# Performance work log

Measured on AMD Instinct MI355X. Metric: run time of the kernel, lower is better.

## Reference

```python
import jax, jax.numpy as jnp
import numpy as np

N_NODES = 50000
N_EDGES = 800000
HIDDEN = 128
IN_DIM = 128
OUT_DIM = 1
N_LAYERS = 4
N_GRAPHS = 32
LN_EPS = 1e-5


def setup_inputs() -> dict:
    key = jax.random.key(0)
    ks = jax.random.split(key, 12)
    s = 1.0 / np.sqrt(HIDDEN)
    inp = {
        "x": jax.random.normal(ks[0], (N_NODES, IN_DIM), dtype=jnp.float32),
        "edge_index": jax.random.randint(ks[1], (2, N_EDGES), 0, N_NODES, dtype=jnp.int64),
        "batch": jnp.sort(jax.random.randint(ks[2], (N_NODES,), 0, N_GRAPHS, dtype=jnp.int64)),
        "W_emb": jax.random.normal(ks[3], (HIDDEN, IN_DIM), dtype=jnp.float32) * s,
        "b_emb": jax.random.normal(ks[4], (HIDDEN,), dtype=jnp.float32) * s,
        "W_layers": jax.random.normal(ks[5], (N_LAYERS, HIDDEN, HIDDEN), dtype=jnp.float32) * s,
        "b_layers": jax.random.normal(ks[6], (N_LAYERS, HIDDEN), dtype=jnp.float32) * s,
        "ln_gamma": 1.0 + 0.02 * jax.random.normal(ks[7], (N_LAYERS, HIDDEN), dtype=jnp.float32),
        "ln_beta": 0.02 * jax.random.normal(ks[8], (N_LAYERS, HIDDEN), dtype=jnp.float32),
        "W_out": jax.random.normal(ks[9], (OUT_DIM, HIDDEN), dtype=jnp.float32) * s,
    }
    return inp


def _layer_norm(x, gamma, beta):
    mu = jnp.mean(x, axis=-1, keepdims=True)
    var = jnp.mean(jnp.square(x - mu), axis=-1, keepdims=True)
    return (x - mu) * jax.lax.rsqrt(var + LN_EPS) * gamma + beta


def reference(x, edge_index, batch, W_emb, b_emb, W_layers, b_layers, ln_gamma, ln_beta, W_out):
    n = x.shape[0]
    # add self-loops (PyG GCNConv default)
    loop = jnp.arange(n, dtype=edge_index.dtype)
    row = jnp.concatenate([edge_index[0], loop])  # source nodes
    col = jnp.concatenate([edge_index[1], loop])  # target nodes
    # symmetric normalization: deg over targets
    deg = jax.ops.segment_sum(jnp.ones_like(col, dtype=x.dtype), col, num_segments=n)
    dis = jnp.where(deg > 0, jax.lax.rsqrt(jnp.maximum(deg, 1.0)), 0.0)
    norm = dis[row] * dis[col]  # [E+N]

    h = x @ W_emb.T + b_emb  # embedding layer
    for i in range(N_LAYERS):
        t = h @ W_layers[i].T                      # [N, H] linear first
        msg = t[row] * norm[:, None]               # gather + scale  [E+N, H]
        agg = jax.ops.segment_sum(msg, col, num_segments=n) + b_layers[i]
        h = _layer_norm(h + jax.nn.relu(agg), ln_gamma[i], ln_beta[i])

    out = h @ W_out.T                              # [N, OUT_DIM]
    sums = jax.ops.segment_sum(out, batch, num_segments=N_GRAPHS)
    cnts = jax.ops.segment_sum(jnp.ones((n,), out.dtype), batch, num_segments=N_GRAPHS)
    return sums / jnp.maximum(cnts, 1.0)[:, None]  # [N_GRAPHS, OUT_DIM]
```

## Files before the change

kernel.cpp:

```cpp
#include <hip/hip_runtime.h>
#include <hip/hip_fp16.h>

#define NN 50000
#define NE 800000
#define NH 128
#define NG 32
#define NL 4
#define NB 196
#define PREPB 320
#define HISTB 3125
#define NTILE 12500
#define WSLOT (NH * NH)

typedef __attribute__((ext_vector_type(8))) short bf16x8;
typedef __attribute__((ext_vector_type(4))) float f32x4;
typedef __attribute__((ext_vector_type(2))) float f32x2;

__device__ inline short f2bf(float x) {
  union { float f; unsigned u; } v;
  v.f = x;
  unsigned r = v.u + 0x7FFF + ((v.u >> 16) & 1);
  return (short)(r >> 16);
}
__device__ inline float bf2f(short s) {
  union { unsigned u; float f; } v;
  v.u = ((unsigned)(unsigned short)s) << 16;
  return v.f;
}

__device__ inline int pdw(int t, int quad) {
  return (((2 * t + (quad >> 1)) & 3) << 3) + ((t >> 1) << 1) + (quad & 1);
}

__device__ inline void fp8row_fma(float (&ag)[4][8], uint4 qa, uint4 qb,
                                  float w) {
  const unsigned dw[8] = {qa.x, qa.y, qa.z, qa.w, qb.x, qb.y, qb.z, qb.w};
#pragma unroll
  for (int ks = 0; ks < 4; ++ks) {
    f32x2 u0 = __builtin_amdgcn_cvt_pk_f32_fp8(dw[2 * ks], 0);
    f32x2 u1 = __builtin_amdgcn_cvt_pk_f32_fp8(dw[2 * ks], 1);
    f32x2 u2 = __builtin_amdgcn_cvt_pk_f32_fp8(dw[2 * ks + 1], 0);
    f32x2 u3 = __builtin_amdgcn_cvt_pk_f32_fp8(dw[2 * ks + 1], 1);
    ag[ks][0] += u0.x * w; ag[ks][1] += u0.y * w;
    ag[ks][2] += u1.x * w; ag[ks][3] += u1.y * w;
    ag[ks][4] += u2.x * w; ag[ks][5] += u2.y * w;
    ag[ks][6] += u3.x * w; ag[ks][7] += u3.y * w;
  }
}

__device__ inline int block_exscan(int v) {
  __shared__ int wsum[4];
  int tid = threadIdx.x, wave = tid >> 6, lane = tid & 63;
  int x = v;
#pragma unroll
  for (int off = 1; off < 64; off <<= 1) {
    int y = __shfl_up(x, off, 64);
    if (lane >= off) x += y;
  }
  if (lane == 63) wsum[wave] = x;
  __syncthreads();
  int wp = 0;
  if (wave > 0) wp += wsum[0];
  if (wave > 1) wp += wsum[1];
  if (wave > 2) wp += wsum[2];
  return wp + x - v;
}

__global__ __launch_bounds__(256) void prep_hist_kernel(
    const float* __restrict__ W_emb, const float* __restrict__ W_layers,
    short* __restrict__ hi, short* __restrict__ lo, const int* __restrict__ row,
    const int* __restrict__ col, int* __restrict__ cnt4,
    int* __restrict__ rank) {
  if (blockIdx.x < PREPB) {
    int i = blockIdx.x * 256 + threadIdx.x;
    if (i >= 5 * WSLOT) return;
    int slot = i >> 14, f = i & (WSLOT - 1);
    int j = f & 7, lane = (f >> 3) & 63, tt = (f >> 9) & 7, ks = f >> 12;
    int n = tt * 16 + (lane & 15);
    int k = ks * 32 + ((lane >> 4) & 3) * 8 + j;
    const float* W = slot ? (W_layers + (size_t)(slot - 1) * WSLOT) : W_emb;
    float x = W[n * NH + k];
    short hh = f2bf(x);
    hi[i] = hh;
    lo[i] = f2bf(x - bf2f(hh));
  } else {
    int e = (blockIdx.x - PREPB) * 256 + threadIdx.x;
    if (e < NE) {
      int s = row[e];
      int t = s / NTILE;
      rank[e] = atomicAdd(&cnt4[col[e] * 4 + t], 1);
    }
  }
}

__global__ __launch_bounds__(256) void scan1_kernel(const int* __restrict__ cnt4,
                                                    int* __restrict__ bsum,
                                                    float* __restrict__ dis,
                                                    int* __restrict__ deg) {
  int i = blockIdx.x * 256 + threadIdx.x;
  int v = 0;
  if (i < NN) {
    int4 c4 = *(const int4*)&cnt4[i * 4];
    v = c4.x + c4.y + c4.z + c4.w;
    deg[i] = v;
    dis[i] = rsqrtf((float)(v + 1));
  }
  int lane = threadIdx.x & 63;
  int s = v;
#pragma unroll
  for (int off = 32; off; off >>= 1) s += __shfl_down(s, off, 64);
  __shared__ int ws[4];
  if (lane == 0) ws[threadIdx.x >> 6] = s;
  __syncthreads();
  if (threadIdx.x == 0) bsum[blockIdx.x] = ws[0] + ws[1] + ws[2] + ws[3];
}

__global__ __launch_bounds__(256) void scan3b_kernel(const int* __restrict__ deg,
                                                     const int* __restrict__ bsum,
                                                     int* __restrict__ offs) {
  __shared__ int ws2[4];
  int tid = threadIdx.x;
  int b = blockIdx.x;
  int v = (tid < NB && tid < b) ? bsum[tid] : 0;
  int lane = tid & 63;
  int s = v;
#pragma unroll
  for (int off = 32; off; off >>= 1) s += __shfl_down(s, off, 64);
  if (lane == 0) ws2[tid >> 6] = s;
  __syncthreads();
  int bo = ws2[0] + ws2[1] + ws2[2] + ws2[3];
  int i = b * 256 + tid;
  int c = (i < NN) ? deg[i] : 0;
  int ex = block_exscan(c);
  if (i < NN) offs[i] = bo + ex;
}

__global__ __launch_bounds__(256) void fill_kernel(const int* __restrict__ row,
                                                   const int* __restrict__ col,
                                                   const int* __restrict__ rank,
                                                   const int* __restrict__ cnt4,
                                                   const float* __restrict__ dis,
                                                   const int* __restrict__ offs,
                                                   int2* __restrict__ csr) {
  int e = blockIdx.x * 256 + threadIdx.x;
  if (e < NE) {
    int d = col[e];
    int s = row[e];
    int t = s / NTILE;
    int4 c4 = *(const int4*)&cnt4[d * 4];
    int pre = (t > 0 ? c4.x : 0) + (t > 1 ? c4.y : 0) + (t > 2 ? c4.z : 0);
    int pos = offs[d] + pre + rank[e];
    csr[pos] = make_int2(s, __float_as_int(dis[s] * dis[d]));
  }
}

__global__ __launch_bounds__(512) void emb_gemm(const float* __restrict__ Xf,
                                                const short* __restrict__ Whi,
                                                const short* __restrict__ Wlo,
                                                const float* __restrict__ bias,
                                                __half* __restrict__ hnew,
                                                unsigned char* __restrict__ h8) {
  __shared__ short Wh[WSLOT];
  __shared__ short Wl[WSLOT];
  int tid = threadIdx.x;
#pragma unroll
  for (int i = tid * 8; i < WSLOT; i += 512 * 8) {
    *(bf16x8*)&Wh[i] = *(const bf16x8*)(Whi + i);
    *(bf16x8*)&Wl[i] = *(const bf16x8*)(Wlo + i);
  }
  __syncthreads();

  int wave = tid >> 6, lane = tid & 63;
  int quad = lane >> 4, r16 = lane & 15;
  int m0 = blockIdx.x * 128 + wave * 16;
  if (m0 >= NN) return;
  int mA = m0 + r16;

  f32x4 acc[8];
#pragma unroll
  for (int t = 0; t < 8; ++t) acc[t] = (f32x4){0.f, 0.f, 0.f, 0.f};

#pragma unroll
  for (int ks = 0; ks < 4; ++ks) {
    int klane = ks * 32 + quad * 8;
    const float* xr = Xf + (size_t)mA * NH + klane;
    float4 a0 = *(const float4*)xr;
    float4 a1 = *(const float4*)(xr + 4);
    float af[8] = {a0.x, a0.y, a0.z, a0.w, a1.x, a1.y, a1.z, a1.w};
    bf16x8 xhi, xlo;
#pragma unroll
    for (int j = 0; j < 8; ++j) {
      short h = f2bf(af[j]);
      xhi[j] = h;
      xlo[j] = f2bf(af[j] - bf2f(h));
    }
#pragma unroll
    for (int t = 0; t < 8; ++t) {
      int fidx = ((ks * 8 + t) * 64 + lane) << 3;
      bf16x8 whi = *(const bf16x8*)&Wh[fidx];
      bf16x8 wlo = *(const bf16x8*)&Wl[fidx];
      acc[t] = __builtin_amdgcn_mfma_f32_16x16x32_bf16(whi, xhi, acc[t], 0, 0, 0);
      acc[t] = __builtin_amdgcn_mfma_f32_16x16x32_bf16(whi, xlo, acc[t], 0, 0, 0);
      acc[t] = __builtin_amdgcn_mfma_f32_16x16x32_bf16(wlo, xhi, acc[t], 0, 0, 0);
    }
  }

  int m = m0 + r16;
  int cb = quad * 4;
#pragma unroll
  for (int t = 0; t < 8; ++t) {
    int ch = t * 16 + cb;
    float4 bb = *(const float4*)(bias + ch);
    float o0 = acc[t][0] + bb.x, o1 = acc[t][1] + bb.y;
    float o2 = acc[t][2] + bb.z, o3 = acc[t][3] + bb.w;
    __half2 p01 = __float22half2_rn(make_float2(o0, o1));
    __half2 p23 = __float22half2_rn(make_float2(o2, o3));
    *(uint2*)(hnew + (size_t)m * NH + ch) =
        make_uint2(*(unsigned*)&p01, *(unsigned*)&p23);
    int v = 0;
    v = __builtin_amdgcn_cvt_pk_fp8_f32(o0, o1, v, 0);
    v = __builtin_amdgcn_cvt_pk_fp8_f32(o2, o3, v, 1);
    ((unsigned*)(h8 + (size_t)m * NH))[pdw(t, quad)] = (unsigned)v;
  }
}

template <bool LAST>
__global__ __launch_bounds__(512) void layer_fused(
    const unsigned char* __restrict__ h8in, const short* __restrict__ Whi,
    const short* __restrict__ Wlo, const float* __restrict__ bias,
    const __half* __restrict__ hprev, const float* __restrict__ gamma,
    const float* __restrict__ beta, const float* __restrict__ Wout,
    const float* __restrict__ dis, const int* __restrict__ offs,
    const int* __restrict__ deg, const int2* __restrict__ csr,
    __half* __restrict__ hnew, unsigned char* __restrict__ h8out,
    float* __restrict__ nodeval) {
  __shared__ short Wh[WSLOT];
  __shared__ short Wl[WSLOT];
  int tid = threadIdx.x;
#pragma unroll
  for (int i = tid * 8; i < WSLOT; i += 512 * 8) {
    *(bf16x8*)&Wh[i] = *(const bf16x8*)(Whi + i);
    *(bf16x8*)&Wl[i] = *(const bf16x8*)(Wlo + i);
  }

  int wave = tid >> 6, lane = tid & 63;
  int quad = lane >> 4, r16 = lane & 15;
  int m0 = blockIdx.x * 128 + wave * 16;
  bool active = m0 < NN;
  int nd = active ? m0 + r16 : 0;

  float ag[4][8];
#pragma unroll
  for (int ks = 0; ks < 4; ++ks)
#pragma unroll
    for (int j = 0; j < 8; ++j) ag[ks][j] = 0.f;

  const char* rbase = (const char*)h8in + quad * 32;
  {
    float dii = dis[nd];
    const uint4* rp = (const uint4*)(rbase + (size_t)nd * NH);
    uint4 qa = rp[0], qb = rp[1];
    fp8row_fma(ag, qa, qb, dii * dii);
  }
  int s0 = offs[nd];
  int e = active ? deg[nd] : 0;
  int j = 0;
  for (; j + 2 <= e; j += 2) {
    int2 p0 = csr[s0 + j], p1 = csr[s0 + j + 1];
    const uint4* r0 = (const uint4*)(rbase + (size_t)p0.x * NH);
    const uint4* r1 = (const uint4*)(rbase + (size_t)p1.x * NH);
    uint4 a0 = r0[0], b0 = r0[1];
    uint4 a1 = r1[0], b1 = r1[1];
    fp8row_fma(ag, a0, b0, __int_as_float(p0.y));
    fp8row_fma(ag, a1, b1, __int_as_float(p1.y));
  }
  if (j < e) {
    int2 p0 = csr[s0 + j];
    const uint4* r0 = (const uint4*)(rbase + (size_t)p0.x * NH);
    uint4 a0 = r0[0], b0 = r0[1];
    fp8row_fma(ag, a0, b0, __int_as_float(p0.y));
  }

  __syncthreads();

  if (!active) return;

  f32x4 acc[8];
#pragma unroll
  for (int t = 0; t < 8; ++t) acc[t] = (f32x4){0.f, 0.f, 0.f, 0.f};

#pragma unroll
  for (int ks = 0; ks < 4; ++ks) {
    bf16x8 xhi, xlo;
#pragma unroll
    for (int q = 0; q < 8; ++q) {
      short hh = f2bf(ag[ks][q]);
      xhi[q] = hh;
      xlo[q] = f2bf(ag[ks][q] - bf2f(hh));
    }
#pragma unroll
    for (int t = 0; t < 8; ++t) {
      int fidx = ((ks * 8 + t) * 64 + lane) << 3;
      bf16x8 whi = *(const bf16x8*)&Wh[fidx];
      bf16x8 wlo = *(const bf16x8*)&Wl[fidx];
      acc[t] = __builtin_amdgcn_mfma_f32_16x16x32_bf16(whi, xhi, acc[t], 0, 0, 0);
      acc[t] = __builtin_amdgcn_mfma_f32_16x16x32_bf16(whi, xlo, acc[t], 0, 0, 0);
      acc[t] = __builtin_amdgcn_mfma_f32_16x16x32_bf16(wlo, xhi, acc[t], 0, 0, 0);
    }
  }

  int m = m0 + r16;
  int cb = quad * 4;
  float vv[8][4];
  float s = 0.f, s2 = 0.f;
#pragma unroll
  for (int t = 0; t < 8; ++t) {
    int ch = t * 16 + cb;
    float4 bb = *(const float4*)(bias + ch);
    uint2 hp = *(const uint2*)(hprev + (size_t)m * NH + ch);
    float2 h01 = __half22float2(*(__half2*)&hp.x);
    float2 h23 = __half22float2(*(__half2*)&hp.y);
    float hv[4] = {h01.x, h01.y, h23.x, h23.y};
    float bb4[4] = {bb.x, bb.y, bb.z, bb.w};
#pragma unroll
    for (int r = 0; r < 4; ++r) {
      float z = fmaxf(acc[t][r] + bb4[r], 0.f);
      float val = hv[r] + z;
      vv[t][r] = val;
      s += val;
      s2 += val * val;
    }
  }
  s += __shfl_xor(s, 16, 64);
  s += __shfl_xor(s, 32, 64);
  s2 += __shfl_xor(s2, 16, 64);
  s2 += __shfl_xor(s2, 32, 64);
  float mean = s * (1.f / 128.f);
  float var = fmaxf(s2 * (1.f / 128.f) - mean * mean, 0.f);
  float inv = rsqrtf(var + 1e-5f);
  float d = 0.f;
#pragma unroll
  for (int t = 0; t < 8; ++t) {
    int ch = t * 16 + cb;
    float4 gv = *(const float4*)(gamma + ch);
    float4 bt = *(const float4*)(beta + ch);
    float o0 = (vv[t][0] - mean) * inv * gv.x + bt.x;
    float o1 = (vv[t][1] - mean) * inv * gv.y + bt.y;
    float o2 = (vv[t][2] - mean) * inv * gv.z + bt.z;
    float o3 = (vv[t][3] - mean) * inv * gv.w + bt.w;
    if (!LAST) {
      __half2 p01 = __float22half2_rn(make_float2(o0, o1));
      __half2 p23 = __float22half2_rn(make_float2(o2, o3));
      *(uint2*)(hnew + (size_t)m * NH + ch) =
          make_uint2(*(unsigned*)&p01, *(unsigned*)&p23);
      int pv = 0;
      pv = __builtin_amdgcn_cvt_pk_fp8_f32(o0, o1, pv, 0);
      pv = __builtin_amdgcn_cvt_pk_fp8_f32(o2, o3, pv, 1);
      ((unsigned*)(h8out + (size_t)m * NH))[pdw(t, quad)] = (unsigned)pv;
    } else {
      float4 wv = *(const float4*)(Wout + ch);
      d += o0 * wv.x + o1 * wv.y + o2 * wv.z + o3 * wv.w;
    }
  }
  if (LAST) {
    d += __shfl_xor(d, 16, 64);
    d += __shfl_xor(d, 32, 64);
    if (lane < 16) nodeval[m] = d;
  }
}

__global__ __launch_bounds__(256) void reduce_pool_kernel(
    const float* __restrict__ nodeval, const int* __restrict__ batch,
    float* __restrict__ gsum, int* __restrict__ gcnt, int* __restrict__ done,
    float* __restrict__ out) {
  __shared__ float bins[NG];
  __shared__ int cbins[NG];
  __shared__ int lastflag;
  int tid = threadIdx.x;
  if (tid < NG) {
    bins[tid] = 0.f;
    cbins[tid] = 0;
  }
  __syncthreads();
  int i = blockIdx.x * 256 + tid;
  if (i < NN) {
    int g = batch[i];
    atomicAdd(&bins[g], nodeval[i]);
    atomicAdd(&cbins[g], 1);
  }
  __syncthreads();
  if (tid < NG && cbins[tid]) {
    atomicAdd(&gsum[tid], bins[tid]);
    atomicAdd(&gcnt[tid], cbins[tid]);
  }
  __threadfence();
  if (tid == 0) lastflag = (atomicAdd(done, 1) == (int)gridDim.x - 1);
  __syncthreads();
  if (lastflag && tid < NG) {
    float sv = atomicAdd(&gsum[tid], 0.f);
    int cv = atomicAdd(&gcnt[tid], 0);
    out[tid] = sv / fmaxf((float)cv, 1.0f);
  }
}

extern "C" void kernel_launch(void* const* d_in, const int* in_sizes, int n_in,
                              void* d_out, int out_size, void* d_ws, size_t ws_size,
                              hipStream_t stream) {
  const float* x = (const float*)d_in[0];
  const int* eidx = (const int*)d_in[1];
  const int* batch = (const int*)d_in[2];
  const float* W_emb = (const float*)d_in[3];
  const float* b_emb = (const float*)d_in[4];
  const float* W_layers = (const float*)d_in[5];
  const float* b_layers = (const float*)d_in[6];
  const float* ln_gamma = (const float*)d_in[7];
  const float* ln_beta = (const float*)d_in[8];
  const float* W_out = (const float*)d_in[9];
  float* out = (float*)d_out;

  char* ws = (char*)d_ws;
  unsigned char* h8a = (unsigned char*)ws; ws += (size_t)NN * NH;
  unsigned char* h8b = (unsigned char*)ws; ws += (size_t)NN * NH;
  __half* h = (__half*)ws;      ws += (size_t)NN * NH * 2;
  short* Whi = (short*)ws;      ws += (size_t)5 * WSLOT * 2;
  short* Wlo = (short*)ws;      ws += (size_t)5 * WSLOT * 2;
  float* dis = (float*)ws;      ws += (size_t)NN * 4;
  int2* csr = (int2*)ws;        ws += (size_t)NE * 8;
  int* rank = (int*)ws;         ws += (size_t)NE * 4;
  int* offs = (int*)ws;         ws += (size_t)NN * 4;
  int* deg = (int*)ws;          ws += (size_t)NN * 4;
  float* nodeval = (float*)ws;  ws += (size_t)NN * 4;
  int* bsum = (int*)ws;         ws += (size_t)NB * 4;
  char* zero_base = ws;
  int* cnt4 = (int*)ws;         ws += (size_t)NN * 16;
  float* gsum = (float*)ws;     ws += (size_t)NG * 4;
  int* gcnt = (int*)ws;         ws += (size_t)NG * 4;
  int* done = (int*)ws;         ws += 64;
  size_t zero_bytes = (size_t)(ws - zero_base);
  hipMemsetAsync(zero_base, 0, zero_bytes, stream);

  const int* erow = eidx;
  const int* ecol = eidx + NE;

  prep_hist_kernel<<<PREPB + HISTB, 256, 0, stream>>>(W_emb, W_layers, Whi, Wlo,
                                                      erow, ecol, cnt4, rank);
  scan1_kernel<<<NB, 256, 0, stream>>>(cnt4, bsum, dis, deg);
  scan3b_kernel<<<NB, 256, 0, stream>>>(deg, bsum, offs);
  fill_kernel<<<HISTB, 256, 0, stream>>>(erow, ecol, rank, cnt4, dis, offs, csr);

  int gblk = (NN + 127) / 128;
  emb_gemm<<<gblk, 512, 0, stream>>>(x, Whi, Wlo, b_emb, h, h8a);
  for (int l = 0; l < NL; ++l) {
    const short* wh = Whi + (size_t)(l + 1) * WSLOT;
    const short* wl = Wlo + (size_t)(l + 1) * WSLOT;
    const float* bl = b_layers + (size_t)l * NH;
    const float* gl = ln_gamma + (size_t)l * NH;
    const float* be = ln_beta + (size_t)l * NH;
    const unsigned char* hin = (l & 1) ? h8b : h8a;
    unsigned char* hout = (l & 1) ? h8a : h8b;
    if (l == NL - 1)
      layer_fused<true><<<gblk, 512, 0, stream>>>(
          hin, wh, wl, bl, h, gl, be, W_out, dis, offs, deg, csr, h, nullptr,
          nodeval);
    else
      layer_fused<false><<<gblk, 512, 0, stream>>>(
          hin, wh, wl, bl, h, gl, be, nullptr, dis, offs, deg, csr, h, hout,
          nullptr);
  }
  reduce_pool_kernel<<<NB, 256, 0, stream>>>(nodeval, batch, gsum, gcnt, done,
                                             out);
}
```

Measured before the change: 327.1 us.

## Split each node's edge gather across four waves and fold self-loops into CSR

The layer kernel now processes 16 nodes per 256-thread block. Each of the four waves gathers a quarter of every node's edge list, and the partial sums are reduced through shared memory before wave 0 runs the MFMA projection. Self-loop entries are written into the CSR by the scan kernel, so the separate self-loop gather and the deg/dis reads are gone. Weights are read straight from global memory instead of being staged in LDS. This gives more parallelism to the latency-bound gather, at the cost of an LDS reduction, three of four waves idling during the GEMM and epilogue, and repeated global weight loads.

```diff
diff --git a/kernel.cpp b/kernel.cpp
--- a/kernel.cpp
+++ b/kernel.cpp
@@ -3,14 +3,17 @@
 
 #define NN 50000
 #define NE 800000
+#define NETOT (NE + NN)
 #define NH 128
 #define NG 32
 #define NL 4
 #define NB 196
 #define PREPB 320
 #define HISTB 3125
+#define GBLK16 3125
 #define NTILE 12500
 #define WSLOT (NH * NH)
+#define PSTR 33
 
 typedef __attribute__((ext_vector_type(8))) short bf16x8;
 typedef __attribute__((ext_vector_type(4))) float f32x4;
@@ -101,9 +104,9 @@
   int v = 0;
   if (i < NN) {
     int4 c4 = *(const int4*)&cnt4[i * 4];
-    v = c4.x + c4.y + c4.z + c4.w;
+    v = c4.x + c4.y + c4.z + c4.w + 1;
     deg[i] = v;
-    dis[i] = rsqrtf((float)(v + 1));
+    dis[i] = rsqrtf((float)v);
   }
   int lane = threadIdx.x & 63;
   int s = v;
@@ -117,7 +120,9 @@
 
 __global__ __launch_bounds__(256) void scan3b_kernel(const int* __restrict__ deg,
                                                      const int* __restrict__ bsum,
-                                                     int* __restrict__ offs) {
+                                                     const float* __restrict__ dis,
+                                                     int* __restrict__ offs,
+                                                     int2* __restrict__ csr) {
   __shared__ int ws2[4];
   int tid = threadIdx.x;
   int b = blockIdx.x;
@@ -132,7 +137,13 @@
   int i = b * 256 + tid;
   int c = (i < NN) ? deg[i] : 0;
   int ex = block_exscan(c);
-  if (i < NN) offs[i] = bo + ex;
+  if (i < NN) {
+    int o = bo + ex;
+    offs[i] = o;
+    float dii = dis[i];
+    csr[o + c - 1] =
+        make_int2((i << 6) | (i & 63), __float_as_int(dii * dii));
+  }
 }
 
 __global__ __launch_bounds__(256) void fill_kernel(const int* __restrict__ row,
@@ -150,7 +161,8 @@
     int4 c4 = *(const int4*)&cnt4[d * 4];
     int pre = (t > 0 ? c4.x : 0) + (t > 1 ? c4.y : 0) + (t > 2 ? c4.z : 0);
     int pos = offs[d] + pre + rank[e];
-    csr[pos] = make_int2(s, __float_as_int(dis[s] * dis[d]));
+    csr[pos] =
+        make_int2((s << 6) | (d & 63), __float_as_int(dis[s] * dis[d]));
   }
 }
 
@@ -225,29 +237,18 @@
 }
 
 template <bool LAST>
-__global__ __launch_bounds__(512) void layer_fused(
+__global__ __launch_bounds__(256) void layer_fused(
     const unsigned char* __restrict__ h8in, const short* __restrict__ Whi,
     const short* __restrict__ Wlo, const float* __restrict__ bias,
     const __half* __restrict__ hprev, const float* __restrict__ gamma,
     const float* __restrict__ beta, const float* __restrict__ Wout,
-    const float* __restrict__ dis, const int* __restrict__ offs,
-    const int* __restrict__ deg, const int2* __restrict__ csr,
+    const int* __restrict__ offs, const int2* __restrict__ csr,
     __half* __restrict__ hnew, unsigned char* __restrict__ h8out,
     float* __restrict__ nodeval) {
-  __shared__ short Wh[WSLOT];
-  __shared__ short Wl[WSLOT];
-  int tid = threadIdx.x;
-#pragma unroll
-  for (int i = tid * 8; i < WSLOT; i += 512 * 8) {
-    *(bf16x8*)&Wh[i] = *(const bf16x8*)(Whi + i);
-    *(bf16x8*)&Wl[i] = *(const bf16x8*)(Wlo + i);
-  }
-
-  int wave = tid >> 6, lane = tid & 63;
+  __shared__ float part_s[3 * 64 * PSTR];
+  int tid = threadIdx.x, wave = tid >> 6, lane = tid & 63;
   int quad = lane >> 4, r16 = lane & 15;
-  int m0 = blockIdx.x * 128 + wave * 16;
-  bool active = m0 < NN;
-  int nd = active ? m0 + r16 : 0;
+  int nd = blockIdx.x * 16 + r16;
 
   float ag[4][8];
 #pragma unroll
@@ -256,34 +257,46 @@
     for (int j = 0; j < 8; ++j) ag[ks][j] = 0.f;
 
   const char* rbase = (const char*)h8in + quad * 32;
-  {
-    float dii = dis[nd];
-    const uint4* rp = (const uint4*)(rbase + (size_t)nd * NH);
-    uint4 qa = rp[0], qb = rp[1];
-    fp8row_fma(ag, qa, qb, dii * dii);
-  }
   int s0 = offs[nd];
-  int e = active ? deg[nd] : 0;
-  int j = 0;
-  for (; j + 2 <= e; j += 2) {
-    int2 p0 = csr[s0 + j], p1 = csr[s0 + j + 1];
-    const uint4* r0 = (const uint4*)(rbase + (size_t)p0.x * NH);
-    const uint4* r1 = (const uint4*)(rbase + (size_t)p1.x * NH);
+  int e1 = (nd + 1 < NN) ? offs[nd + 1] : NETOT;
+  int deg = e1 - s0;
+  int q0 = s0 + ((deg * wave) >> 2);
+  int q1 = s0 + ((deg * (wave + 1)) >> 2);
+  int j = q0;
+  for (; j + 2 <= q1; j += 2) {
+    int2 p0 = csr[j], p1 = csr[j + 1];
+    const uint4* r0 = (const uint4*)(rbase + (size_t)(((unsigned)p0.x) >> 6) * NH);
+    const uint4* r1 = (const uint4*)(rbase + (size_t)(((unsigned)p1.x) >> 6) * NH);
     uint4 a0 = r0[0], b0 = r0[1];
     uint4 a1 = r1[0], b1 = r1[1];
     fp8row_fma(ag, a0, b0, __int_as_float(p0.y));
     fp8row_fma(ag, a1, b1, __int_as_float(p1.y));
   }
-  if (j < e) {
-    int2 p0 = csr[s0 + j];
-    const uint4* r0 = (const uint4*)(rbase + (size_t)p0.x * NH);
+  if (j < q1) {
+    int2 p0 = csr[j];
+    const uint4* r0 = (const uint4*)(rbase + (size_t)(((unsigned)p0.x) >> 6) * NH);
     uint4 a0 = r0[0], b0 = r0[1];
     fp8row_fma(ag, a0, b0, __int_as_float(p0.y));
   }
 
-  __syncthreads();
-
-  if (!active) return;
+  if (wave != 0) {
+    int base = ((wave - 1) * 64 + lane) * PSTR;
+#pragma unroll
+    for (int ks = 0; ks < 4; ++ks)
+#pragma unroll
+      for (int q = 0; q < 8; ++q) part_s[base + ks * 8 + q] = ag[ks][q];
+  }
+  __syncthreads();
+  if (wave != 0) return;
+
+#pragma unroll
+  for (int w2 = 0; w2 < 3; ++w2) {
+    int base = (w2 * 64 + lane) * PSTR;
+#pragma unroll
+    for (int ks = 0; ks < 4; ++ks)
+#pragma unroll
+      for (int q = 0; q < 8; ++q) ag[ks][q] += part_s[base + ks * 8 + q];
+  }
 
   f32x4 acc[8];
 #pragma unroll
@@ -301,15 +314,15 @@
 #pragma unroll
     for (int t = 0; t < 8; ++t) {
       int fidx = ((ks * 8 + t) * 64 + lane) << 3;
-      bf16x8 whi = *(const bf16x8*)&Wh[fidx];
-      bf16x8 wlo = *(const bf16x8*)&Wl[fidx];
+      bf16x8 whi = *(const bf16x8*)&Whi[fidx];
+      bf16x8 wlo = *(const bf16x8*)&Wlo[fidx];
       acc[t] = __builtin_amdgcn_mfma_f32_16x16x32_bf16(whi, xhi, acc[t], 0, 0, 0);
       acc[t] = __builtin_amdgcn_mfma_f32_16x16x32_bf16(whi, xlo, acc[t], 0, 0, 0);
       acc[t] = __builtin_amdgcn_mfma_f32_16x16x32_bf16(wlo, xhi, acc[t], 0, 0, 0);
     }
   }
 
-  int m = m0 + r16;
+  int m = nd;
   int cb = quad * 4;
   float vv[8][4];
   float s = 0.f, s2 = 0.f;
@@ -425,7 +438,7 @@
   short* Whi = (short*)ws;      ws += (size_t)5 * WSLOT * 2;
   short* Wlo = (short*)ws;      ws += (size_t)5 * WSLOT * 2;
   float* dis = (float*)ws;      ws += (size_t)NN * 4;
-  int2* csr = (int2*)ws;        ws += (size_t)NE * 8;
+  int2* csr = (int2*)ws;        ws += (size_t)NETOT * 8;
   int* rank = (int*)ws;         ws += (size_t)NE * 4;
   int* offs = (int*)ws;         ws += (size_t)NN * 4;
   int* deg = (int*)ws;          ws += (size_t)NN * 4;
@@ -445,7 +458,7 @@
   prep_hist_kernel<<<PREPB + HISTB, 256, 0, stream>>>(W_emb, W_layers, Whi, Wlo,
                                                       erow, ecol, cnt4, rank);
   scan1_kernel<<<NB, 256, 0, stream>>>(cnt4, bsum, dis, deg);
-  scan3b_kernel<<<NB, 256, 0, stream>>>(deg, bsum, offs);
+  scan3b_kernel<<<NB, 256, 0, stream>>>(deg, bsum, dis, offs, csr);
   fill_kernel<<<HISTB, 256, 0, stream>>>(erow, ecol, rank, cnt4, dis, offs, csr);
 
   int gblk = (NN + 127) / 128;
@@ -459,13 +472,11 @@
     const unsigned char* hin = (l & 1) ? h8b : h8a;
     unsigned char* hout = (l & 1) ? h8a : h8b;
     if (l == NL - 1)
-      layer_fused<true><<<gblk, 512, 0, stream>>>(
-          hin, wh, wl, bl, h, gl, be, W_out, dis, offs, deg, csr, h, nullptr,
-          nodeval);
+      layer_fused<true><<<GBLK16, 256, 0, stream>>>(
+          hin, wh, wl, bl, h, gl, be, W_out, offs, csr, h, nullptr, nodeval);
     else
-      layer_fused<false><<<gblk, 512, 0, stream>>>(
-          hin, wh, wl, bl, h, gl, be, nullptr, dis, offs, deg, csr, h, hout,
-          nullptr);
+      layer_fused<false><<<GBLK16, 256, 0, stream>>>(
+          hin, wh, wl, bl, h, gl, be, nullptr, offs, csr, h, hout, nullptr);
   }
   reduce_pool_kernel<<<NB, 256, 0, stream>>>(nodeval, batch, gsum, gcnt, done,
                                              out);
```

Result: slower. 432.8 us (+32.3%).
